# Kernel tuning notes

Measured on AMD Instinct MI355X. Metric: run time of the kernel, lower is better.

Reference implementation:

```python
import jax, jax.numpy as jnp
import numpy as np

V, E, H, T, B = 33278, 400, 1150, 128, 32
LAYER_DIMS = [(E, H), (H, H), (H, E)]  # (input, hidden) per layer; last tied -> E


def _uniform(key, shape, scale):
    return jax.random.uniform(key, shape, jnp.float32, -scale, scale)


def setup_inputs() -> dict:
    key = jax.random.key(0)
    ks = jax.random.split(key, 20)
    inp = {
        'input': jax.random.randint(ks[0], (T, B), 0, V),
        'emb_W': _uniform(ks[1], (V, E), 0.1),
        'final_b': jnp.zeros((V,), jnp.float32),
    }
    ki = 2
    for l, (din, dh) in enumerate(LAYER_DIMS):
        s = 1.0 / np.sqrt(dh)
        inp[f'Wih_l{l}'] = _uniform(ks[ki + 0], (4 * dh, din), s)
        inp[f'Whh_l{l}'] = _uniform(ks[ki + 1], (4 * dh, dh), s)
        inp[f'bih_l{l}'] = _uniform(ks[ki + 2], (4 * dh,), s)
        inp[f'bhh_l{l}'] = _uniform(ks[ki + 3], (4 * dh,), s)
        ki += 4
        inp[f'h0_l{l}'] = jnp.zeros((B, dh), jnp.float32)
        inp[f'c0_l{l}'] = jnp.zeros((B, dh), jnp.float32)
    return inp


def lstm_layer(x, h0, c0, Wih, Whh, bih, bhh):
    # x: [T, B, din]; PyTorch gate order i, f, g, o
    xg = jnp.einsum('tbi,gi->tbg', x, Wih) + bih  # [T, B, 4H]

    def step(carry, xg_t):
        h, c = carry
        g = xg_t + h @ Whh.T + bhh
        i, f, gg, o = jnp.split(g, 4, axis=-1)
        c = jax.nn.sigmoid(f) * c + jax.nn.sigmoid(i) * jnp.tanh(gg)
        h = jax.nn.sigmoid(o) * jnp.tanh(c)
        return (h, c), h

    (hT, cT), ys = jax.lax.scan(step, (h0, c0), xg)
    return ys, hT, cT


def reference(input, emb_W, final_b,
              Wih_l0, Whh_l0, bih_l0, bhh_l0,
              Wih_l1, Whh_l1, bih_l1, bhh_l1,
              Wih_l2, Whh_l2, bih_l2, bhh_l2,
              h0_l0, c0_l0, h0_l1, c0_l1, h0_l2, c0_l2):
    # Eval-mode AWD-LSTM encoder: all dropouts are identity.
    x = emb_W[input]  # [T, B, E]
    params = [(Wih_l0, Whh_l0, bih_l0, bhh_l0, h0_l0, c0_l0),
              (Wih_l1, Whh_l1, bih_l1, bhh_l1, h0_l1, c0_l1),
              (Wih_l2, Whh_l2, bih_l2, bhh_l2, h0_l2, c0_l2)]
    new_hidden = []
    for (Wih, Whh, bih, bhh, h0, c0) in params:
        x, hT, cT = lstm_layer(x, h0, c0, Wih, Whh, bih, bhh)
        new_hidden.extend([hT, cT])
    # Tied decoder: final.weight = embedding.weight ([V, E])
    logits = jnp.einsum('tbe,ve->tbv', x, emb_W) + final_b  # [T, B, V]
    return (logits, *new_hidden)
```

## Files before the change

### kernel.cpp

```cpp
#include <hip/hip_runtime.h>
#include <math.h>

#define T_ 128
#define B_ 32
#define V_ 33278
#define E_ 400

typedef __bf16 bf16x8 __attribute__((ext_vector_type(8)));
typedef float f32x4 __attribute__((ext_vector_type(4)));

#define AGENT_LD(p) __hip_atomic_load((p), __ATOMIC_RELAXED, __HIP_MEMORY_SCOPE_AGENT)
#define AGENT_ST(p, v) __hip_atomic_store((p), (v), __ATOMIC_RELAXED, __HIP_MEMORY_SCOPE_AGENT)

__device__ __forceinline__ float exp2f_(float x) {
  float r;
  asm("v_exp_f32 %0, %1" : "=v"(r) : "v"(x));
  return r;
}
__device__ __forceinline__ float rcpf_(float x) {
  float r;
  asm("v_rcp_f32 %0, %1" : "=v"(r) : "v"(x));
  return r;
}
__device__ __forceinline__ float sigf_(float x) { return rcpf_(1.0f + exp2f_(-1.44269504f * x)); }
__device__ __forceinline__ float tanhf_(float x) {
  float t = exp2f_(2.88539008f * x);
  return 1.0f - 2.0f * rcpf_(t + 1.0f);
}

__device__ __forceinline__ unsigned short f2bf(float f) {
  unsigned u = __float_as_uint(f);
  unsigned lsb = (u >> 16) & 1;
  return (unsigned short)((u + 0x7FFFu + lsb) >> 16);
}

__device__ __forceinline__ void gload16(const unsigned short* g, unsigned short* l) {
  __builtin_amdgcn_global_load_lds((const __attribute__((address_space(1))) void*)g,
                                   (__attribute__((address_space(3))) void*)l, 16, 0, 0);
}

__global__ void embed_kernel(const int* __restrict__ idx, const float* __restrict__ W,
                             unsigned short* __restrict__ x) {
  int i = blockIdx.x * blockDim.x + threadIdx.x;
  if (i >= T_ * B_ * 416) return;
  int k = i % 416;
  int tb = i / 416;
  x[i] = (k < E_) ? f2bf(W[(size_t)idx[tb] * E_ + k]) : 0;
}

__global__ void convW(const float* __restrict__ in, unsigned short* __restrict__ out, int N, int K,
                      int Kp, long total) {
  long i = (long)blockIdx.x * blockDim.x + threadIdx.x;
  if (i >= total) return;
  int k = (int)(i % Kp);
  long n = i / Kp;
  out[i] = (n < N && k < K) ? f2bf(in[n * (long)K + k]) : 0;
}

__global__ __launch_bounds__(256) void gemm_bf16(const unsigned short* __restrict__ A,
                                                 const unsigned short* __restrict__ B,
                                                 const float* __restrict__ bias0,
                                                 const float* __restrict__ bias1,
                                                 float* __restrict__ C, int M, int Kp, int ldc,
                                                 int realN, int gateN) {
  __shared__ __align__(16) unsigned short lsA[4 * 128 * 8];
  __shared__ __align__(16) unsigned short lsB[4 * 128 * 8];
  const int tid = threadIdx.x;
  const int lane = tid & 63;
  const int w = tid >> 6;
  const int wm = (w >> 1) * 64;
  const int wn = (w & 1) * 64;
  const int lr = lane & 15;
  const int kq = lane >> 4;
  const int m0 = blockIdx.y * 128;
  const int n0 = blockIdx.x * 128;

  f32x4 acc[4][4] = {};

  const int kiters = Kp >> 5;
  for (int kt = 0; kt < kiters; ++kt) {
    const int k0 = kt << 5;
#pragma unroll
    for (int q = 0; q < 2; ++q) {
      int s = w + q * 4;
      int kc = s >> 1, rb = (s & 1) * 64;
      gload16(A + (size_t)(m0 + rb + lane) * Kp + k0 + kc * 8, lsA + s * 512);
      gload16(B + (size_t)(n0 + rb + lane) * Kp + k0 + kc * 8, lsB + s * 512);
    }
    __syncthreads();

    bf16x8 af[4], bf[4];
#pragma unroll
    for (int mf = 0; mf < 4; ++mf)
      af[mf] = *(const bf16x8*)&lsA[(kq * 128 + wm + mf * 16 + lr) * 8];
#pragma unroll
    for (int nf = 0; nf < 4; ++nf)
      bf[nf] = *(const bf16x8*)&lsB[(kq * 128 + wn + nf * 16 + lr) * 8];
#pragma unroll
    for (int mf = 0; mf < 4; ++mf)
#pragma unroll
      for (int nf = 0; nf < 4; ++nf)
        acc[mf][nf] = __builtin_amdgcn_mfma_f32_16x16x32_bf16(af[mf], bf[nf], acc[mf][nf], 0, 0, 0);
    __syncthreads();
  }

#pragma unroll
  for (int nf = 0; nf < 4; ++nf) {
    int n = n0 + wn + nf * 16 + lr;
    if (n >= realN) continue;
    float bsum = 0.0f;
    if (bias0) bsum += bias0[n];
    if (bias1) bsum += bias1[n];
    int col = n;
    if (gateN > 0) {
      int g = (n >= gateN) + (n >= 2 * gateN) + (n >= 3 * gateN);
      int u = n - g * gateN;
      col = u * 4 + g;
    }
#pragma unroll
    for (int mf = 0; mf < 4; ++mf) {
      int mbase = m0 + wm + mf * 16 + kq * 4;
#pragma unroll
      for (int r = 0; r < 4; ++r) C[(size_t)(mbase + r) * ldc + col] = acc[mf][nf][r] + bsum;
    }
  }
}


struct FP {
  const float* xg0;
  float* ring;
  const unsigned short *whh0, *wih1, *whh1, *wih2, *whh2;
  const float *h0_0, *c0_0, *h0_1, *c0_1, *h0_2, *c0_2;
  const float *bih1, *bhh1, *bih2, *bhh2;
  unsigned short *xc1, *xc2, *xc3;
  float *oh0, *oc0, *oh1, *oc1, *oh2, *oc2;
  int* flags;
};

__device__ __forceinline__ void pollset(const int* f, int hf, int n, int tgt) {
  int lane = threadIdx.x & 63;
  for (;;) {
    int v = (lane < n) ? AGENT_LD(&f[((lane << 1) + hf) * 16]) : tgt;
    if (__all(v >= tgt)) break;
  }
}

template <int KT>
__device__ __forceinline__ void stage(const unsigned short* slab, unsigned short* lds) {
  constexpr int KP = KT * 32, KPP = KP + 8, U64R = KP / 4, NCH = 16 * U64R;
  constexpr int NIT = (NCH + 511) / 512;
  const int tid = threadIdx.x;
  unsigned long long d[NIT];
#pragma unroll
  for (int i = 0; i < NIT; ++i) {
    int c = tid + i * 512;
    if (c < NCH)
      d[i] = AGENT_LD((const unsigned long long*)(slab + (size_t)(c / U64R) * KP) + (c % U64R));
  }
#pragma unroll
  for (int i = 0; i < NIT; ++i) {
    int c = tid + i * 512;
    if (c < NCH) *(unsigned long long*)&lds[(c / U64R) * KPP + (c % U64R) * 4] = d[i];
  }
}

template <int KT>
__device__ __forceinline__ void load_aw(const unsigned short* w, int dh, int U0, int wv, int lm,
                                        int kq, bf16x8* aw) {
  const int ga = lm & 3, ula = lm >> 2;
  const int ua = U0 + wv * 4 + ula;
  const unsigned short* wr = w + (size_t)(ga * dh + (ua < dh ? ua : 0)) * (KT * 32);
#pragma unroll
  for (int kt = 0; kt < KT; ++kt) aw[kt] = *(const bf16x8*)&wr[kt * 32 + kq * 8];
}

template <int KT>
__device__ __forceinline__ void mm4(const bf16x8* aw, const unsigned short* lds, int lm, int kq,
                                    f32x4& a0, f32x4& a1, f32x4& a2, f32x4& a3) {
  constexpr int KPP = KT * 32 + 8;
  const unsigned short* rp = lds + lm * KPP + kq * 8;
#pragma unroll
  for (int kt = 0; kt < KT; kt += 4) {
    a0 = __builtin_amdgcn_mfma_f32_16x16x32_bf16(aw[kt], *(const bf16x8*)&rp[kt * 32], a0, 0, 0, 0);
    if (kt + 1 < KT)
      a1 = __builtin_amdgcn_mfma_f32_16x16x32_bf16(aw[kt + 1], *(const bf16x8*)&rp[(kt + 1) * 32],
                                                   a1, 0, 0, 0);
    if (kt + 2 < KT)
      a2 = __builtin_amdgcn_mfma_f32_16x16x32_bf16(aw[kt + 2], *(const bf16x8*)&rp[(kt + 2) * 32],
                                                   a2, 0, 0, 0);
    if (kt + 3 < KT)
      a3 = __builtin_amdgcn_mfma_f32_16x16x32_bf16(aw[kt + 3], *(const bf16x8*)&rp[(kt + 3) * 32],
                                                   a3, 0, 0, 0);
  }
}

__device__ __forceinline__ void pub_h(unsigned short* dst, float hn, bool vu, int kq) {
  unsigned hv = vu ? (unsigned)f2bf(hn) : 0u;
  unsigned t16 = (unsigned)__shfl_xor((int)hv, 16);
  unsigned v32 = (kq & 1) ? (t16 | (hv << 16)) : (hv | (t16 << 16));
  unsigned o32 = (unsigned)__shfl_xor((int)v32, 32);
  if (kq == 0)
    AGENT_ST((unsigned long long*)dst, (unsigned long long)v32 | ((unsigned long long)o32 << 32));
}

__global__ __launch_bounds__(512, 2) void fused_lstm(FP P) {
  __shared__ __align__(16) unsigned short sbuf[16 * 1160 + 16 * 424];
  const int tid = threadIdx.x;
  const int lane = tid & 63;
  const int wv = tid >> 6;
  const int lm = lane & 15;
  const int kq = lane >> 4;
  const int bid = blockIdx.x;
  int* f0 = P.flags;
  int* fh = P.flags + 72 * 16;
  int* f1 = P.flags + 144 * 16;
  int* f2 = P.flags + 216 * 16;

  if (bid < 72) {
    constexpr int KT = 36, KP = 1152;
    const int hf = bid & 1, gid = bid >> 1, U0 = gid * 32;
    const int gb = hf * 16 + lm, un = U0 + wv * 4 + kq;
    const bool vu = un < 1150;
    bf16x8 aw[KT];
    load_aw<KT>(P.whh0, 1150, U0, wv, lm, kq, aw);
    float creg = vu ? P.c0_0[gb * 1150 + un] : 0.f;
    pub_h(P.xc1 + (size_t)gb * KP + U0 + wv * 4, vu ? P.h0_0[gb * 1150 + un] : 0.f, vu, kq);
    asm volatile("s_waitcnt vmcnt(0)" ::: "memory");
    __syncthreads();
    if (tid == 0) AGENT_ST(&f0[(gid * 2 + hf) * 16], 1);
    for (int t = 0; t < T_; ++t) {
      f32x4 cinit = *(const f32x4*)&P.xg0[(size_t)(t * 32 + gb) * 4608 + un * 4];
      if (wv == 0) pollset(f0, hf, 36, t + 1);
      else if (wv == 1 && t >= 8) pollset(f1, hf, 36, t - 7);
      __syncthreads();
      stage<KT>(P.xc1 + (size_t)(t * 32 + hf * 16) * KP, sbuf);
      __syncthreads();
      f32x4 a0 = cinit, a1 = {0.f, 0.f, 0.f, 0.f}, a2 = {0.f, 0.f, 0.f, 0.f},
            a3 = {0.f, 0.f, 0.f, 0.f};
      mm4<KT>(aw, sbuf, lm, kq, a0, a1, a2, a3);
      float gi = a0[0] + a1[0] + a2[0] + a3[0], gf = a0[1] + a1[1] + a2[1] + a3[1];
      float gg = a0[2] + a1[2] + a2[2] + a3[2], go = a0[3] + a1[3] + a2[3] + a3[3];
      float cn = sigf_(gf) * creg + sigf_(gi) * tanhf_(gg);
      float hn = sigf_(go) * tanhf_(cn);
      creg = cn;
      pub_h(P.xc1 + (size_t)((t + 1) * 32 + gb) * KP + U0 + wv * 4, hn, vu, kq);
      if (t == T_ - 1 && vu) { P.oh0[gb * 1150 + un] = hn; P.oc0[gb * 1150 + un] = cn; }
      asm volatile("s_waitcnt vmcnt(0)" ::: "memory");
      __syncthreads();
      if (tid == 0) AGENT_ST(&f0[(gid * 2 + hf) * 16], t + 2);
    }
  } else if (bid < 144) {
    constexpr int KT = 36, KP = 1152;
    const int idx = bid - 72, hf = idx & 1, gid = idx >> 1, U0 = gid * 32;
    const int gb = hf * 16 + lm, un = U0 + wv * 4 + kq;
    const bool vu = un < 1150;
    bf16x8 aw[KT];
    load_aw<KT>(P.wih1, 1150, U0, wv, lm, kq, aw);
    f32x4 bini = {0.f, 0.f, 0.f, 0.f};
    if (vu) {
#pragma unroll
      for (int g = 0; g < 4; ++g) bini[g] = P.bih1[g * 1150 + un] + P.bhh1[g * 1150 + un];
    }
    for (int t = 0; t < T_; ++t) {
      if (wv == 0) pollset(f0, hf, 36, t + 2);
      __syncthreads();
      stage<KT>(P.xc1 + (size_t)((t + 1) * 32 + hf * 16) * KP, sbuf);
      __syncthreads();
      f32x4 a0 = bini, a1 = {0.f, 0.f, 0.f, 0.f}, a2 = {0.f, 0.f, 0.f, 0.f},
            a3 = {0.f, 0.f, 0.f, 0.f};
      mm4<KT>(aw, sbuf, lm, kq, a0, a1, a2, a3);
      float r0 = a0[0] + a1[0] + a2[0] + a3[0], r1 = a0[1] + a1[1] + a2[1] + a3[1];
      float r2 = a0[2] + a1[2] + a2[2] + a3[2], r3 = a0[3] + a1[3] + a2[3] + a3[3];
      unsigned long long* dst =
          (unsigned long long*)(P.ring + ((size_t)(t & 15) * 32 + gb) * 4608 + un * 4);
      AGENT_ST(dst, ((unsigned long long)__float_as_uint(r1) << 32) | __float_as_uint(r0));
      AGENT_ST(dst + 1, ((unsigned long long)__float_as_uint(r3) << 32) | __float_as_uint(r2));
      asm volatile("s_waitcnt vmcnt(0)" ::: "memory");
      __syncthreads();
      if (tid == 0) AGENT_ST(&fh[(gid * 2 + hf) * 16], t + 1);
    }
  } else if (bid < 216) {
    constexpr int KT = 36, KP = 1152;
    const int idx = bid - 144, hf = idx & 1, gid = idx >> 1, U0 = gid * 32;
    const int gb = hf * 16 + lm, un = U0 + wv * 4 + kq;
    const bool vu = un < 1150;
    bf16x8 aw[KT];
    load_aw<KT>(P.whh1, 1150, U0, wv, lm, kq, aw);
    float creg = vu ? P.c0_1[gb * 1150 + un] : 0.f;
    pub_h(P.xc2 + (size_t)gb * KP + U0 + wv * 4, vu ? P.h0_1[gb * 1150 + un] : 0.f, vu, kq);
    asm volatile("s_waitcnt vmcnt(0)" ::: "memory");
    __syncthreads();
    if (tid == 0) AGENT_ST(&f1[(gid * 2 + hf) * 16], 1);
    for (int t = 0; t < T_; ++t) {
      if (wv == 0) pollset(f1, hf, 36, t + 1);
      else if (wv == 1) {
        for (;;) {
          int v = AGENT_LD(&fh[(gid * 2 + hf) * 16]);
          if (__all(v >= t + 1)) break;
        }
      }
      __syncthreads();
      stage<KT>(P.xc2 + (size_t)(t * 32 + hf * 16) * KP, sbuf);
      const unsigned long long* rp =
          (const unsigned long long*)(P.ring + ((size_t)(t & 15) * 32 + gb) * 4608 + un * 4);
      unsigned long long q0 = AGENT_LD(rp), q1 = AGENT_LD(rp + 1);
      __syncthreads();
      f32x4 a0, a1 = {0.f, 0.f, 0.f, 0.f}, a2 = {0.f, 0.f, 0.f, 0.f}, a3 = {0.f, 0.f, 0.f, 0.f};
      a0[0] = __uint_as_float((unsigned)q0);
      a0[1] = __uint_as_float((unsigned)(q0 >> 32));
      a0[2] = __uint_as_float((unsigned)q1);
      a0[3] = __uint_as_float((unsigned)(q1 >> 32));
      mm4<KT>(aw, sbuf, lm, kq, a0, a1, a2, a3);
      float gi = a0[0] + a1[0] + a2[0] + a3[0], gf = a0[1] + a1[1] + a2[1] + a3[1];
      float gg = a0[2] + a1[2] + a2[2] + a3[2], go = a0[3] + a1[3] + a2[3] + a3[3];
      float cn = sigf_(gf) * creg + sigf_(gi) * tanhf_(gg);
      float hn = sigf_(go) * tanhf_(cn);
      creg = cn;
      pub_h(P.xc2 + (size_t)((t + 1) * 32 + gb) * KP + U0 + wv * 4, hn, vu, kq);
      if (t == T_ - 1 && vu) { P.oh1[gb * 1150 + un] = hn; P.oc1[gb * 1150 + un] = cn; }
      asm volatile("s_waitcnt vmcnt(0)" ::: "memory");
      __syncthreads();
      if (tid == 0) AGENT_ST(&f1[(gid * 2 + hf) * 16], t + 2);
    }
  } else {
    constexpr int KTA = 36, KPA = 1152, KTB = 13, KPB = 416;
    const int idx = bid - 216, hf = idx & 1, gid = idx >> 1, U0 = gid * 32;
    const int gb = hf * 16 + lm, un = U0 + wv * 4 + kq;
    const bool vu = un < 400;
    bf16x8 awi[KTA];
    load_aw<KTA>(P.wih2, 400, U0, wv, lm, kq, awi);
    bf16x8 awh[KTB];
    load_aw<KTB>(P.whh2, 400, U0, wv, lm, kq, awh);
    f32x4 bini = {0.f, 0.f, 0.f, 0.f};
    if (vu) {
#pragma unroll
      for (int g = 0; g < 4; ++g) bini[g] = P.bih2[g * 400 + un] + P.bhh2[g * 400 + un];
    }
    float creg = vu ? P.c0_2[gb * 400 + un] : 0.f;
    pub_h(P.xc3 + (size_t)gb * KPB + U0 + wv * 4, vu ? P.h0_2[gb * 400 + un] : 0.f, vu, kq);
    asm volatile("s_waitcnt vmcnt(0)" ::: "memory");
    __syncthreads();
    if (tid == 0) AGENT_ST(&f2[(gid * 2 + hf) * 16], 1);
    unsigned short* h1buf = sbuf;
    unsigned short* h2buf = sbuf + 16 * (KPA + 8);
    for (int t = 0; t < T_; ++t) {
      if (wv == 0) pollset(f1, hf, 36, t + 2);
      else if (wv == 1) pollset(f2, hf, 13, t + 1);
      __syncthreads();
      stage<KTA>(P.xc2 + (size_t)((t + 1) * 32 + hf * 16) * KPA, h1buf);
      stage<KTB>(P.xc3 + (size_t)(t * 32 + hf * 16) * KPB, h2buf);
      __syncthreads();
      f32x4 a0 = bini, a1 = {0.f, 0.f, 0.f, 0.f}, a2 = {0.f, 0.f, 0.f, 0.f},
            a3 = {0.f, 0.f, 0.f, 0.f};
      mm4<KTA>(awi, h1buf, lm, kq, a0, a1, a2, a3);
      mm4<KTB>(awh, h2buf, lm, kq, a0, a1, a2, a3);
      float gi = a0[0] + a1[0] + a2[0] + a3[0], gf = a0[1] + a1[1] + a2[1] + a3[1];
      float gg = a0[2] + a1[2] + a2[2] + a3[2], go = a0[3] + a1[3] + a2[3] + a3[3];
      float cn = sigf_(gf) * creg + sigf_(gi) * tanhf_(gg);
      float hn = sigf_(go) * tanhf_(cn);
      creg = cn;
      pub_h(P.xc3 + (size_t)((t + 1) * 32 + gb) * KPB + U0 + wv * 4, hn, vu, kq);
      if (t == T_ - 1 && vu) { P.oh2[gb * 400 + un] = hn; P.oc2[gb * 400 + un] = cn; }
      asm volatile("s_waitcnt vmcnt(0)" ::: "memory");
      __syncthreads();
      if (tid == 0) AGENT_ST(&f2[(gid * 2 + hf) * 16], t + 2);
    }
  }
}

extern "C" void kernel_launch(void* const* d_in, const int* in_sizes, int n_in, void* d_out,
                              int out_size, void* d_ws, size_t ws_size, hipStream_t stream) {
  const int* input = (const int*)d_in[0];
  const float* emb_W = (const float*)d_in[1];
  const float* final_b = (const float*)d_in[2];

  struct L {
    const float *Wih, *Whh, *bih, *bhh, *h0, *c0;
  };
  L ls[3];
  ls[0] = {(const float*)d_in[3],  (const float*)d_in[4],  (const float*)d_in[5],
           (const float*)d_in[6],  (const float*)d_in[7],  (const float*)d_in[8]};
  ls[1] = {(const float*)d_in[9],  (const float*)d_in[10], (const float*)d_in[11],
           (const float*)d_in[12], (const float*)d_in[13], (const float*)d_in[14]};
  ls[2] = {(const float*)d_in[15], (const float*)d_in[16], (const float*)d_in[17],
           (const float*)d_in[18], (const float*)d_in[19], (const float*)d_in[20]};

  char* base = (char*)d_ws;
  int* flags = (int*)base;
  float* xg0 = (float*)(base + 65536);
  float* ring = xg0 + (size_t)4096 * 4608;
  unsigned short* embbf = (unsigned short*)(ring + (size_t)16 * 32 * 4608);
  unsigned short* w0 = embbf + (size_t)33280 * 416;
  unsigned short* wih1 = w0 + (size_t)4608 * 416;
  unsigned short* whh0 = wih1 + (size_t)4608 * 1152;
  unsigned short* whh1 = whh0 + (size_t)4600 * 1152;
  unsigned short* wih2 = whh1 + (size_t)4600 * 1152;
  unsigned short* whh2 = wih2 + (size_t)1600 * 1152;
  unsigned short* xemb = whh2 + (size_t)1600 * 416;
  unsigned short* xc1 = xemb + (size_t)4096 * 416;
  unsigned short* xc2 = xc1 + (size_t)4128 * 1152;
  unsigned short* xc3 = xc2 + (size_t)4128 * 1152;
  float* out = (float*)d_out;

  hipMemsetAsync(flags, 0, 65536, stream);

  {
    long tot = (long)33280 * 416;
    convW<<<(unsigned)((tot + 255) / 256), 256, 0, stream>>>(emb_W, embbf, V_, E_, 416, tot);
  }
  {
    long tot = (long)4608 * 416;
    convW<<<(unsigned)((tot + 255) / 256), 256, 0, stream>>>(ls[0].Wih, w0, 4600, 400, 416, tot);
  }
  {
    long tot = (long)4608 * 1152;
    convW<<<(unsigned)((tot + 255) / 256), 256, 0, stream>>>(ls[1].Wih, wih1, 4600, 1150, 1152,
                                                             tot);
  }
  {
    long tot = (long)4600 * 1152;
    convW<<<(unsigned)((tot + 255) / 256), 256, 0, stream>>>(ls[0].Whh, whh0, 4600, 1150, 1152,
                                                             tot);
    convW<<<(unsigned)((tot + 255) / 256), 256, 0, stream>>>(ls[1].Whh, whh1, 4600, 1150, 1152,
                                                             tot);
  }
  {
    long tot = (long)1600 * 1152;
    convW<<<(unsigned)((tot + 255) / 256), 256, 0, stream>>>(ls[2].Wih, wih2, 1600, 1150, 1152,
                                                             tot);
  }
  {
    long tot = (long)1600 * 416;
    convW<<<(unsigned)((tot + 255) / 256), 256, 0, stream>>>(ls[2].Whh, whh2, 1600, 400, 416, tot);
  }
  embed_kernel<<<(T_ * B_ * 416 + 255) / 256, 256, 0, stream>>>(input, emb_W, xemb);

  long o = (long)T_ * B_ * V_;
  float* oh0 = out + o;
  float* oc0 = oh0 + 32 * 1150;
  float* oh1 = oc0 + 32 * 1150;
  float* oc1 = oh1 + 32 * 1150;
  float* oh2 = oc1 + 32 * 1150;
  float* oc2 = oh2 + 32 * 400;

  gemm_bf16<<<dim3(36, 32), 256, 0, stream>>>(xemb, w0, ls[0].bih, ls[0].bhh, xg0, 4096, 416, 4608,
                                              4600, 1150);

  FP P;
  P.xg0 = xg0;
  P.ring = ring;
  P.whh0 = whh0;
  P.wih1 = wih1;
  P.whh1 = whh1;
  P.wih2 = wih2;
  P.whh2 = whh2;
  P.h0_0 = ls[0].h0;
  P.c0_0 = ls[0].c0;
  P.h0_1 = ls[1].h0;
  P.c0_1 = ls[1].c0;
  P.h0_2 = ls[2].h0;
  P.c0_2 = ls[2].c0;
  P.bih1 = ls[1].bih;
  P.bhh1 = ls[1].bhh;
  P.bih2 = ls[2].bih;
  P.bhh2 = ls[2].bhh;
  P.xc1 = xc1;
  P.xc2 = xc2;
  P.xc3 = xc3;
  P.oh0 = oh0;
  P.oc0 = oc0;
  P.oh1 = oh1;
  P.oc1 = oc1;
  P.oh2 = oh2;
  P.oc2 = oc2;
  P.flags = flags;
  fused_lstm<<<242, 512, 0, stream>>>(P);

  gemm_bf16<<<dim3(260, 32), 256, 0, stream>>>(xc3 + (size_t)32 * 416, embbf, final_b, nullptr,
                                               out, 4096, 416, V_, V_, 0);
}
```

Baseline: 1.573 ms.

## Reuse xg buffer for layer-1 projections, drop ring backpressure, widen staging loads

The layer-1 input-projection blocks now write their results into the already-consumed time slot of the layer-0 xg buffer instead of a 16-slot ring. This removes the backpressure poll in which layer 0 waited on layer 1. Hidden-state staging switches from 8-byte agent-scope atomic loads to plain 16-byte vector loads, and layer 2 issues both slabs' loads before its LDS writes. Spin loops gain s_sleep to reduce polling pressure on memory. The risks are stale-cache reads from the non-atomic loads and slightly higher wake-up latency from the sleeps.

```diff
diff --git a/kernel.cpp b/kernel.cpp
--- a/kernel.cpp
+++ b/kernel.cpp
@@ -128,8 +128,7 @@
 
 
 struct FP {
-  const float* xg0;
-  float* ring;
+  float* xg;
   const unsigned short *whh0, *wih1, *whh1, *wih2, *whh2;
   const float *h0_0, *c0_0, *h0_1, *c0_1, *h0_2, *c0_2;
   const float *bih1, *bhh1, *bih2, *bhh2;
@@ -143,25 +142,64 @@
   for (;;) {
     int v = (lane < n) ? AGENT_LD(&f[((lane << 1) + hf) * 16]) : tgt;
     if (__all(v >= tgt)) break;
+    __builtin_amdgcn_s_sleep(1);
+  }
+}
+
+__device__ __forceinline__ void pollone(const int* f, int tgt) {
+  for (;;) {
+    int v = AGENT_LD(f);
+    if (__all(v >= tgt)) break;
+    __builtin_amdgcn_s_sleep(1);
   }
 }
 
 template <int KT>
 __device__ __forceinline__ void stage(const unsigned short* slab, unsigned short* lds) {
-  constexpr int KP = KT * 32, KPP = KP + 8, U64R = KP / 4, NCH = 16 * U64R;
+  constexpr int KP = KT * 32, KPP = KP + 8, C16 = KP / 8, NCH = 16 * C16;
   constexpr int NIT = (NCH + 511) / 512;
   const int tid = threadIdx.x;
-  unsigned long long d[NIT];
+  uint4 d[NIT];
 #pragma unroll
   for (int i = 0; i < NIT; ++i) {
     int c = tid + i * 512;
-    if (c < NCH)
-      d[i] = AGENT_LD((const unsigned long long*)(slab + (size_t)(c / U64R) * KP) + (c % U64R));
+    if (c < NCH) d[i] = *(const uint4*)(slab + (size_t)(c / C16) * KP + (c % C16) * 8);
   }
 #pragma unroll
   for (int i = 0; i < NIT; ++i) {
     int c = tid + i * 512;
-    if (c < NCH) *(unsigned long long*)&lds[(c / U64R) * KPP + (c % U64R) * 4] = d[i];
+    if (c < NCH) *(uint4*)&lds[(c / C16) * KPP + (c % C16) * 8] = d[i];
+  }
+}
+
+template <int KTA, int KTB>
+__device__ __forceinline__ void stage2(const unsigned short* slabA, const unsigned short* slabB,
+                                       unsigned short* ldsA, unsigned short* ldsB) {
+  constexpr int KPA = KTA * 32, KPPA = KPA + 8, CA = KPA / 8, NA = 16 * CA;
+  constexpr int NITA = (NA + 511) / 512;
+  constexpr int KPB = KTB * 32, KPPB = KPB + 8, CB = KPB / 8, NB = 16 * CB;
+  constexpr int NITB = (NB + 511) / 512;
+  const int tid = threadIdx.x;
+  uint4 dA[NITA], dB[NITB];
+#pragma unroll
+  for (int i = 0; i < NITA; ++i) {
+    int c = tid + i * 512;
+    if (c < NA) dA[i] = *(const uint4*)(slabA + (size_t)(c / CA) * KPA + (c % CA) * 8);
+  }
+#pragma unroll
+  for (int i = 0; i < NITB; ++i) {
+    int c = tid + i * 512;
+    if (c < NB) dB[i] = *(const uint4*)(slabB + (size_t)(c / CB) * KPB + (c % CB) * 8);
+  }
+#pragma unroll
+  for (int i = 0; i < NITA; ++i) {
+    int c = tid + i * 512;
+    if (c < NA) *(uint4*)&ldsA[(c / CA) * KPPA + (c % CA) * 8] = dA[i];
+  }
+#pragma unroll
+  for (int i = 0; i < NITB; ++i) {
+    int c = tid + i * 512;
+    if (c < NB) *(uint4*)&ldsB[(c / CB) * KPPB + (c % CB) * 8] = dB[i];
   }
 }
 
@@ -230,9 +268,8 @@
     __syncthreads();
     if (tid == 0) AGENT_ST(&f0[(gid * 2 + hf) * 16], 1);
     for (int t = 0; t < T_; ++t) {
-      f32x4 cinit = *(const f32x4*)&P.xg0[(size_t)(t * 32 + gb) * 4608 + un * 4];
+      f32x4 cinit = *(const f32x4*)&P.xg[(size_t)(t * 32 + gb) * 4608 + un * 4];
       if (wv == 0) pollset(f0, hf, 36, t + 1);
-      else if (wv == 1 && t >= 8) pollset(f1, hf, 36, t - 7);
       __syncthreads();
       stage<KT>(P.xc1 + (size_t)(t * 32 + hf * 16) * KP, sbuf);
       __syncthreads();
@@ -273,7 +310,7 @@
       float r0 = a0[0] + a1[0] + a2[0] + a3[0], r1 = a0[1] + a1[1] + a2[1] + a3[1];
       float r2 = a0[2] + a1[2] + a2[2] + a3[2], r3 = a0[3] + a1[3] + a2[3] + a3[3];
       unsigned long long* dst =
-          (unsigned long long*)(P.ring + ((size_t)(t & 15) * 32 + gb) * 4608 + un * 4);
+          (unsigned long long*)(P.xg + (size_t)(t * 32 + gb) * 4608 + un * 4);
       AGENT_ST(dst, ((unsigned long long)__float_as_uint(r1) << 32) | __float_as_uint(r0));
       AGENT_ST(dst + 1, ((unsigned long long)__float_as_uint(r3) << 32) | __float_as_uint(r2));
       asm volatile("s_waitcnt vmcnt(0)" ::: "memory");
@@ -294,16 +331,11 @@
     if (tid == 0) AGENT_ST(&f1[(gid * 2 + hf) * 16], 1);
     for (int t = 0; t < T_; ++t) {
       if (wv == 0) pollset(f1, hf, 36, t + 1);
-      else if (wv == 1) {
-        for (;;) {
-          int v = AGENT_LD(&fh[(gid * 2 + hf) * 16]);
-          if (__all(v >= t + 1)) break;
-        }
-      }
+      else if (wv == 1) pollone(&fh[(gid * 2 + hf) * 16], t + 1);
       __syncthreads();
       stage<KT>(P.xc2 + (size_t)(t * 32 + hf * 16) * KP, sbuf);
       const unsigned long long* rp =
-          (const unsigned long long*)(P.ring + ((size_t)(t & 15) * 32 + gb) * 4608 + un * 4);
+          (const unsigned long long*)(P.xg + (size_t)(t * 32 + gb) * 4608 + un * 4);
       unsigned long long q0 = AGENT_LD(rp), q1 = AGENT_LD(rp + 1);
       __syncthreads();
       f32x4 a0, a1 = {0.f, 0.f, 0.f, 0.f}, a2 = {0.f, 0.f, 0.f, 0.f}, a3 = {0.f, 0.f, 0.f, 0.f};
@@ -348,8 +380,8 @@
       if (wv == 0) pollset(f1, hf, 36, t + 2);
       else if (wv == 1) pollset(f2, hf, 13, t + 1);
       __syncthreads();
-      stage<KTA>(P.xc2 + (size_t)((t + 1) * 32 + hf * 16) * KPA, h1buf);
-      stage<KTB>(P.xc3 + (size_t)(t * 32 + hf * 16) * KPB, h2buf);
+      stage2<KTA, KTB>(P.xc2 + (size_t)((t + 1) * 32 + hf * 16) * KPA,
+                       P.xc3 + (size_t)(t * 32 + hf * 16) * KPB, h1buf, h2buf);
       __syncthreads();
       f32x4 a0 = bini, a1 = {0.f, 0.f, 0.f, 0.f}, a2 = {0.f, 0.f, 0.f, 0.f},
             a3 = {0.f, 0.f, 0.f, 0.f};
@@ -389,8 +421,7 @@
   char* base = (char*)d_ws;
   int* flags = (int*)base;
   float* xg0 = (float*)(base + 65536);
-  float* ring = xg0 + (size_t)4096 * 4608;
-  unsigned short* embbf = (unsigned short*)(ring + (size_t)16 * 32 * 4608);
+  unsigned short* embbf = (unsigned short*)(xg0 + (size_t)4096 * 4608);
   unsigned short* w0 = embbf + (size_t)33280 * 416;
   unsigned short* wih1 = w0 + (size_t)4608 * 416;
   unsigned short* whh0 = wih1 + (size_t)4608 * 1152;
@@ -448,8 +479,7 @@
                                               4600, 1150);
 
   FP P;
-  P.xg0 = xg0;
-  P.ring = ring;
+  P.xg = xg0;
   P.whh0 = whh0;
   P.wih1 = wih1;
   P.whh1 = whh1;
```

Measured after the change: 1.576 ms. About the same (+0.2%).
